# Kernel optimization log

Hardware: AMD Instinct MI355X
Metric: run time of the kernel (lower is better)

Reference implementation:

```python
import jax, jax.numpy as jnp
import numpy as np

N_NODES = 100000
N_EDGES = 1600000
IN_F = 64
OUT_F = 64
GRID_SIZE = 5
SPLINE_ORDER = 3
GRID_MIN, GRID_MAX = -1.0, 1.0
N_COEF = GRID_SIZE + SPLINE_ORDER  # 8 spline coefficients per (in,out)


def make_grid():
    # Extended knot grid, shape (IN_F, GRID_SIZE + 2*SPLINE_ORDER + 1)
    h = (GRID_MAX - GRID_MIN) / GRID_SIZE
    pts = jnp.arange(-SPLINE_ORDER, GRID_SIZE + SPLINE_ORDER + 1, dtype=jnp.float32) * h + GRID_MIN
    return jnp.tile(pts[None, :], (IN_F, 1))


def b_splines(x, grid):
    # x: (N, IN_F) -> bases: (N, IN_F, N_COEF) via Cox-de Boor recursion
    xe = x[..., None]
    bases = ((xe >= grid[:, :-1]) & (xe < grid[:, 1:])).astype(x.dtype)
    for j in range(1, SPLINE_ORDER + 1):
        left = (xe - grid[:, : -(j + 1)]) / (grid[:, j:-1] - grid[:, : -(j + 1)])
        right = (grid[:, j + 1:] - xe) / (grid[:, j + 1:] - grid[:, 1:-j])
        bases = left * bases[..., :-1] + right * bases[..., 1:]
    return bases


def kan_apply(x, base_w, spline_w, grid):
    # base path: silu(x) @ W_b^T ; spline path: flattened B-spline bases @ W_s^T
    base = jnp.matmul(jax.nn.silu(x), base_w.T)
    sp = b_splines(x, grid).reshape(x.shape[0], -1)          # (N, IN_F*N_COEF)
    spline = jnp.matmul(sp, spline_w.reshape(OUT_F, -1).T)    # (N, OUT_F)
    return base + spline


def setup_inputs() -> dict:
    key = jax.random.key(0)
    k1, k2, k3, k4, k5, k6 = jax.random.split(key, 6)
    x = jax.random.normal(k1, (N_NODES, IN_F), dtype=jnp.float32)
    edge_index = jax.random.randint(k2, (2, N_EDGES), 0, N_NODES, dtype=jnp.int32)
    s = 1.0 / np.sqrt(IN_F)
    base_w_layer = jax.random.normal(k3, (OUT_F, IN_F), dtype=jnp.float32) * s
    spline_w_layer = jax.random.normal(k4, (OUT_F, IN_F, N_COEF), dtype=jnp.float32) * 0.1 * s
    base_w_conv = jax.random.normal(k5, (OUT_F, IN_F), dtype=jnp.float32) * s
    spline_w_conv = jax.random.normal(k6, (OUT_F, IN_F, N_COEF), dtype=jnp.float32) * 0.1 * s
    return {
        "x": x,
        "base_w_layer": base_w_layer,
        "spline_w_layer": spline_w_layer,
        "base_w_conv": base_w_conv,
        "spline_w_conv": spline_w_conv,
        "edge_index": edge_index,
    }


def reference(x, base_w_layer, spline_w_layer, base_w_conv, spline_w_conv, edge_index):
    grid = make_grid()
    src, dst = edge_index[0], edge_index[1]
    # A_hat symmetric normalization: deg^{-1/2}[src] * deg^{-1/2}[dst]
    deg = jax.ops.segment_sum(jnp.ones(src.shape[0], x.dtype), dst, num_segments=N_NODES)
    dinv = jnp.where(deg > 0, jax.lax.rsqrt(jnp.maximum(deg, 1.0)), 0.0)
    coef = dinv[src] * dinv[dst]                              # (E,)
    msg = x[src] * coef[:, None]                              # (E, IN_F) gather
    agg = jax.ops.segment_sum(msg, dst, num_segments=N_NODES) # (N, IN_F) scatter-add
    # aggregate_first=True: KAN transform applied after aggregation
    h_layer = kan_apply(x, base_w_layer, spline_w_layer, grid)
    h_conv = kan_apply(agg, base_w_conv, spline_w_conv, grid)
    return h_layer + h_conv
```

## Files before the change

kernel.cpp:

```cpp
#include <hip/hip_runtime.h>
#include <math.h>

#define N_NODES 100000
#define N_EDGES 1600000
#define IN_F 64
#define OUT_F 64

#define K_SLOT 10
#define CH_IF 16
#define AST 172
#define AGH 33
#define NB 64
#define NTHR 256
#define EMAXW 448

#define NBUCK 256
#define NBUCK_USED 196
#define BSH 9
#define BCAP 9728
#define BUCK_N 512
#define EPT 8
#define EPB 2048

#define NODES_PAD 100352
#define WF_U16 (8 * 20 * 512)
#define WG_SLOTS (WF_U16 / 2)
#define CSR_CAP (NBUCK_USED * BCAP)
#define OFF_DINV 0
#define OFF_ROWPTR (OFF_DINV + NODES_PAD)
#define OFF_ROWEND (OFF_ROWPTR + NODES_PAD)
#define OFF_WT (OFF_ROWEND + NODES_PAD)
#define OFF_BF (OFF_WT + WG_SLOTS)
#define OFF_CSR (OFF_BF + 256)
#define FIXED_SLOTS (OFF_CSR + CSR_CAP)
#define XH_SLOTS (N_NODES * IN_F / 2)
#define OFF_XH FIXED_SLOTS
#define FIXED2 (FIXED_SLOTS + XH_SLOTS)
#define AGG_ELEMS (N_NODES * IN_F)

typedef __attribute__((ext_vector_type(8))) short bf16x8;
typedef __attribute__((ext_vector_type(4))) short bf16x4;
typedef __attribute__((ext_vector_type(4))) float f32x4;

__device__ __forceinline__ unsigned int bf16_rne(float v) {
    unsigned int u = __float_as_uint(v);
    u += 0x7FFFu + ((u >> 16) & 1u);
    return u >> 16;
}

__global__ __launch_bounds__(256)
void bucket_bin_kernel(const int* __restrict__ ei, int* __restrict__ bf,
                       int2* __restrict__ pairs) {
    __shared__ int lh[NBUCK];
    __shared__ int lbs[NBUCK];
    __shared__ int lgb[NBUCK];
    __shared__ int2 spair[EPB];
    __shared__ int  sdst[EPB];
    int t = threadIdx.x;
    lh[t] = 0;
    __syncthreads();
    int e0 = blockIdx.x * EPB;
    int nE = N_EDGES - e0; if (nE > EPB) nE = EPB; if (nE < 0) nE = 0;
    int d[EPT], s[EPT], lp[EPT];
#pragma unroll
    for (int k = 0; k < EPT; ++k) {
        int idx = k * 256 + t;
        bool ok = idx < nE;
        int e = e0 + idx;
        d[k] = ok ? ei[N_EDGES + e] : -1;
        s[k] = ok ? ei[e] : 0;
        lp[k] = ok ? atomicAdd(&lh[d[k] >> BSH], 1) : 0;
    }
    __syncthreads();
    int v = lh[t];
    lbs[t] = v;
    __syncthreads();
    for (int off = 1; off < NBUCK; off <<= 1) {
        int add = (t >= off) ? lbs[t - off] : 0;
        __syncthreads();
        lbs[t] += add;
        __syncthreads();
    }
    int excl = lbs[t] - v;
    if (v) {
        int r = atomicAdd(&bf[t], v);
        int cap = (t + 1) * BCAP - v;
        lgb[t] = r > cap ? cap : r;
    }
    __syncthreads();
    lbs[t] = excl;
    __syncthreads();
#pragma unroll
    for (int k = 0; k < EPT; ++k) {
        if (d[k] >= 0) {
            int b = d[k] >> BSH;
            int sp = lbs[b] + lp[k];
            spair[sp] = make_int2(d[k], s[k]);
            sdst[sp] = lgb[b] + lp[k];
        }
    }
    __syncthreads();
    for (int p = t; p < nE; p += 256) pairs[sdst[p]] = spair[p];
}

__global__ __launch_bounds__(BUCK_N)
void bucket_build_kernel(const int2* __restrict__ pairs, const int* __restrict__ bf,
                         int* __restrict__ rowptr, int* __restrict__ rowend,
                         float* __restrict__ dinv, int* __restrict__ csr,
                         const float* __restrict__ x, unsigned short* __restrict__ xh) {
    __shared__ int ldeg[BUCK_N];
    __shared__ int sb[BUCK_N];
    __shared__ int lpos[BUCK_N];
    int t = threadIdx.x;
    int b = blockIdx.x;
    int base = b * BCAP;
    int cnt = bf[b] - base;
    if (cnt > BCAP) cnt = BCAP;
    ldeg[t] = 0;
    __syncthreads();
    for (int j = t; j < cnt; j += BUCK_N) atomicAdd(&ldeg[pairs[base + j].x & (BUCK_N - 1)], 1);
    __syncthreads();
    int v = ldeg[t];
    sb[t] = v;
    __syncthreads();
    for (int off = 1; off < BUCK_N; off <<= 1) {
        int add = (t >= off) ? sb[t - off] : 0;
        __syncthreads();
        sb[t] += add;
        __syncthreads();
    }
    int excl = sb[t] - v;
    int node = (b << BSH) + t;
    if (node < N_NODES) {
        rowptr[node] = base + excl;
        rowend[node] = base + excl + v;
        dinv[node] = (v > 0) ? rsqrtf((float)v) : 0.0f;
    }
    lpos[t] = base + excl;
    __syncthreads();
    for (int j = t; j < cnt; j += BUCK_N) {
        int2 p = pairs[base + j];
        int pos = atomicAdd(&lpos[p.x & (BUCK_N - 1)], 1);
        csr[pos] = p.y;
    }
    if (xh) {
        int nodebase = b << BSH;
        for (int f = t; f < BUCK_N * 16; f += BUCK_N) {
            int nl = f >> 4;
            int nd = nodebase + nl;
            if (nd < N_NODES) {
                int dg = ldeg[nl];
                float dn = (dg > 0) ? rsqrtf((float)dg) : 0.0f;
                float4 vv = *(const float4*)&x[nd * 64 + (f & 15) * 4];
                uint2 u;
                u.x = bf16_rne(vv.x * dn) | (bf16_rne(vv.y * dn) << 16);
                u.y = bf16_rne(vv.z * dn) | (bf16_rne(vv.w * dn) << 16);
                *(uint2*)&xh[nd * 64 + (f & 15) * 4] = u;
            }
        }
    }
}

__global__ __launch_bounds__(256)
void gather_kernel(const float* __restrict__ x, const int* __restrict__ csr,
                   const int* __restrict__ rowptr, const int* __restrict__ rowend,
                   const float* __restrict__ dinv, float* __restrict__ agg) {
    int wid = (int)((blockIdx.x * 256 + threadIdx.x) >> 6);
    int lane = threadIdx.x & 63;
    if (wid >= N_NODES) return;
    int start = rowptr[wid];
    int end = rowend[wid];
    float acc = 0.0f;
    int j = start;
    for (; j + 3 < end; j += 4) {
        int s0 = csr[j], s1 = csr[j + 1], s2 = csr[j + 2], s3 = csr[j + 3];
        float a0 = x[s0 * 64 + lane] * dinv[s0];
        float a1 = x[s1 * 64 + lane] * dinv[s1];
        float a2 = x[s2 * 64 + lane] * dinv[s2];
        float a3 = x[s3 * 64 + lane] * dinv[s3];
        acc += a0 + a1 + a2 + a3;
    }
    for (; j < end; ++j) {
        int s = csr[j];
        acc += x[s * 64 + lane] * dinv[s];
    }
    agg[wid * 64 + lane] = acc * dinv[wid];
}

__global__ void deg_kernel(const int* __restrict__ ei, float* __restrict__ deg) {
    int e = blockIdx.x * blockDim.x + threadIdx.x;
    if (e < N_EDGES) atomicAdd(&deg[ei[N_EDGES + e]], 1.0f);
}
__global__ void dinv_kernel(float* __restrict__ deg) {
    int n = blockIdx.x * blockDim.x + threadIdx.x;
    if (n < N_NODES) {
        float d = deg[n];
        deg[n] = (d > 0.0f) ? rsqrtf(d) : 0.0f;
    }
}
__global__ void scatter_kernel(const float* __restrict__ x, const int* __restrict__ ei,
                               const float* __restrict__ dinv, float* __restrict__ agg) {
    long long gtid = (long long)blockIdx.x * blockDim.x + threadIdx.x;
    int wid = (int)(gtid >> 6);
    int lane = threadIdx.x & 63;
    if (wid >= N_EDGES) return;
    int s = ei[wid];
    int d = ei[N_EDGES + wid];
    float c = dinv[s] * dinv[d];
    atomicAdd(&agg[d * 64 + lane], x[s * 64 + lane] * c);
}

__global__ void wprep_kernel(const float* __restrict__ bwl, const float* __restrict__ swl,
                             const float* __restrict__ bwc, const float* __restrict__ swc,
                             unsigned short* __restrict__ Wf, int* __restrict__ bf) {
    int gid = blockIdx.x * blockDim.x + threadIdx.x;
    if (bf && gid < NBUCK) bf[gid] = gid * BCAP;
    if (gid >= WF_U16) return;
    int fr = gid >> 9;
    int lj = gid & 511;
    int lane = lj >> 3, j = lj & 7;
    int ch = fr / 20, r2 = fr - ch * 20;
    int s = r2 >> 2, t = r2 & 3;
    int o = t * 16 + (lane & 15);
    int kk = ((lane >> 4) << 3) + s * 32 + j;
    int iL = kk / K_SLOT, c = kk - iL * K_SLOT;
    int i = (ch & 3) * CH_IF + iL;
    int path = ch >> 2;
    const float* bw = path ? bwc : bwl;
    const float* sw = path ? swc : swl;
    float v = 0.0f;
    if (c == 8) v = bw[o * IN_F + i];
    else if (c < 8) v = sw[o * 512 + i * 8 + c];
    Wf[gid] = (unsigned short)bf16_rne(v);
}

__device__ __forceinline__ void write_feat(unsigned short* Arow, int iL, float v) {
    unsigned int* Au = (unsigned int*)(Arow + iL * K_SLOT);
    float sig = __builtin_amdgcn_rcpf(1.0f + __expf(-v));
    Au[0] = 0u; Au[1] = 0u; Au[2] = 0u; Au[3] = 0u;
    Au[4] = bf16_rne(v * sig);
    float s5 = (v + 2.2f) * 2.5f;
    float fm = floorf(s5);
    int m = (int)fm;
    if (m >= 0 && m <= 10) {
        float t = s5 - fm;
        float omt = 1.0f - t;
        float t2 = t * t, t3 = t2 * t;
        float n0 = omt * omt * omt * (1.0f / 6.0f);
        float n3 = t3 * (1.0f / 6.0f);
        float n1 = 0.66666666f - t2 + 0.5f * t3;
        float n2 = 1.0f - n0 - n1 - n3;
        unsigned short* As = Arow + iL * K_SLOT;
        if (m >= 3)           As[m - 3] = (unsigned short)bf16_rne(n0);
        if (m >= 2 && m <= 9) As[m - 2] = (unsigned short)bf16_rne(n1);
        if (m >= 1 && m <= 8) As[m - 1] = (unsigned short)bf16_rne(n2);
        if (m <= 7)           As[m]     = (unsigned short)bf16_rne(n3);
    }
}

__global__ __launch_bounds__(NTHR, 4)
void kan_fused_kernel(const float* __restrict__ x, const unsigned short* __restrict__ xh,
                      const int* __restrict__ csr, const int* __restrict__ rowptr,
                      const int* __restrict__ rowend, const float* __restrict__ dinv,
                      const unsigned short* __restrict__ Wf, float* __restrict__ out) {
    __shared__ __align__(16) unsigned short A_lds[NB * AST];
    __shared__ unsigned int agg_lds[NB * AGH];
    __shared__ int csr_lds[4 * EMAXW];

    int tid = threadIdx.x;
    int nbase = blockIdx.x * NB;
    int wid = tid >> 6;
    int lane = tid & 63;
    int nloc0 = (wid << 4) + (lane & 15);
    int q = lane >> 4;
    int node0 = nbase + nloc0;
    bool ok0 = node0 < N_NODES;

    const float4 z4 = make_float4(0.f, 0.f, 0.f, 0.f);
    float4 vx[4];
#pragma unroll
    for (int c = 0; c < 4; ++c)
        vx[c] = ok0 ? *(const float4*)&x[node0 * 64 + c * CH_IF + q * 4] : z4;

    int wn0 = nbase + (wid << 4);
    int s0w = 0, slenw = 0;
    int* wcsr = &csr_lds[wid * EMAXW];
    if (wn0 < N_NODES) {
        int wnL = wn0 + 15;
        if (wnL >= N_NODES) wnL = N_NODES - 1;
        s0w = rowptr[wn0];
        slenw = rowend[wnL] - s0w;
        int cap = slenw < EMAXW ? slenw : EMAXW;
        for (int i = lane; i < cap; i += 64) wcsr[i] = csr[s0w + i];
    }

    f32x4 acc[4];
#pragma unroll
    for (int t = 0; t < 4; ++t) acc[t] = (f32x4){0.f, 0.f, 0.f, 0.f};

    int kfrag = (lane >> 4) * 8;
    const unsigned short* Abase = &A_lds[nloc0 * AST + kfrag];
    unsigned short* Arow = &A_lds[nloc0 * AST];
    const bf16x8* Bbase = (const bf16x8*)Wf + lane;

    auto do_chunk = [&](int chunk) {
        float vv[4];
        if (chunk < 4) {
            vv[0] = vx[chunk].x; vv[1] = vx[chunk].y; vv[2] = vx[chunk].z; vv[3] = vx[chunk].w;
        } else {
            int b2 = (chunk - 4) * 8 + q * 2;
            unsigned u0 = agg_lds[nloc0 * AGH + b2];
            unsigned u1 = agg_lds[nloc0 * AGH + b2 + 1];
            vv[0] = __uint_as_float(u0 << 16);
            vv[1] = __uint_as_float(u0 & 0xFFFF0000u);
            vv[2] = __uint_as_float(u1 << 16);
            vv[3] = __uint_as_float(u1 & 0xFFFF0000u);
        }
#pragma unroll
        for (int jj = 0; jj < 4; ++jj) write_feat(Arow, q * 4 + jj, vv[jj]);
#pragma unroll
        for (int s = 0; s < 5; ++s) {
            bf16x4 alo = *(const bf16x4*)(Abase + s * 32);
            bf16x4 ahi = *(const bf16x4*)(Abase + s * 32 + 4);
            bf16x8 a = __builtin_shufflevector(alo, ahi, 0, 1, 2, 3, 4, 5, 6, 7);
#pragma unroll
            for (int t = 0; t < 4; ++t) {
                bf16x8 b = Bbase[((chunk * 5 + s) * 4 + t) * 64];
                acc[t] = __builtin_amdgcn_mfma_f32_16x16x32_bf16(a, b, acc[t], 0, 0, 0);
            }
        }
    };

    auto do_gather = [&]() {
        int grp8 = lane >> 3;
        int l8 = lane & 7;
        const uint4* xh128 = (const uint4*)xh;
        for (int p = 0; p < 2; ++p) {
            int nloc = (wid << 4) + (p << 3) + grp8;
            int nd = nbase + nloc;
            float a0 = 0.f, a1 = 0.f, a2 = 0.f, a3 = 0.f;
            float a4 = 0.f, a5 = 0.f, a6 = 0.f, a7 = 0.f;
            float dn = 0.f;
            if (nd < N_NODES) {
                dn = dinv[nd];
                int j = rowptr[nd] - s0w;
                int end = rowend[nd] - s0w;
                if (end <= EMAXW) {
                    for (; j + 15 < end; j += 16) {
                        int sa[16]; uint4 ua[16];
#pragma unroll
                        for (int k = 0; k < 16; ++k) sa[k] = wcsr[j + k];
#pragma unroll
                        for (int k = 0; k < 16; ++k) ua[k] = xh128[sa[k] * 8 + l8];
#pragma unroll
                        for (int k = 0; k < 16; ++k) {
                            a0 += __uint_as_float(ua[k].x << 16);
                            a1 += __uint_as_float(ua[k].x & 0xFFFF0000u);
                            a2 += __uint_as_float(ua[k].y << 16);
                            a3 += __uint_as_float(ua[k].y & 0xFFFF0000u);
                            a4 += __uint_as_float(ua[k].z << 16);
                            a5 += __uint_as_float(ua[k].z & 0xFFFF0000u);
                            a6 += __uint_as_float(ua[k].w << 16);
                            a7 += __uint_as_float(ua[k].w & 0xFFFF0000u);
                        }
                    }
                    for (; j + 3 < end; j += 4) {
                        int sb0 = wcsr[j], sb1 = wcsr[j + 1], sb2 = wcsr[j + 2], sb3 = wcsr[j + 3];
                        uint4 u0 = xh128[sb0 * 8 + l8], u1 = xh128[sb1 * 8 + l8];
                        uint4 u2 = xh128[sb2 * 8 + l8], u3 = xh128[sb3 * 8 + l8];
                        a0 += __uint_as_float(u0.x << 16) + __uint_as_float(u1.x << 16)
                            + __uint_as_float(u2.x << 16) + __uint_as_float(u3.x << 16);
                        a1 += __uint_as_float(u0.x & 0xFFFF0000u) + __uint_as_float(u1.x & 0xFFFF0000u)
                            + __uint_as_float(u2.x & 0xFFFF0000u) + __uint_as_float(u3.x & 0xFFFF0000u);
                        a2 += __uint_as_float(u0.y << 16) + __uint_as_float(u1.y << 16)
                            + __uint_as_float(u2.y << 16) + __uint_as_float(u3.y << 16);
                        a3 += __uint_as_float(u0.y & 0xFFFF0000u) + __uint_as_float(u1.y & 0xFFFF0000u)
                            + __uint_as_float(u2.y & 0xFFFF0000u) + __uint_as_float(u3.y & 0xFFFF0000u);
                        a4 += __uint_as_float(u0.z << 16) + __uint_as_float(u1.z << 16)
                            + __uint_as_float(u2.z << 16) + __uint_as_float(u3.z << 16);
                        a5 += __uint_as_float(u0.z & 0xFFFF0000u) + __uint_as_float(u1.z & 0xFFFF0000u)
                            + __uint_as_float(u2.z & 0xFFFF0000u) + __uint_as_float(u3.z & 0xFFFF0000u);
                        a6 += __uint_as_float(u0.w << 16) + __uint_as_float(u1.w << 16)
                            + __uint_as_float(u2.w << 16) + __uint_as_float(u3.w << 16);
                        a7 += __uint_as_float(u0.w & 0xFFFF0000u) + __uint_as_float(u1.w & 0xFFFF0000u)
                            + __uint_as_float(u2.w & 0xFFFF0000u) + __uint_as_float(u3.w & 0xFFFF0000u);
                    }
                    for (; j < end; ++j) {
                        uint4 u = xh128[wcsr[j] * 8 + l8];
                        a0 += __uint_as_float(u.x << 16);
                        a1 += __uint_as_float(u.x & 0xFFFF0000u);
                        a2 += __uint_as_float(u.y << 16);
                        a3 += __uint_as_float(u.y & 0xFFFF0000u);
                        a4 += __uint_as_float(u.z << 16);
                        a5 += __uint_as_float(u.z & 0xFFFF0000u);
                        a6 += __uint_as_float(u.w << 16);
                        a7 += __uint_as_float(u.w & 0xFFFF0000u);
                    }
                } else {
                    for (int g = rowptr[nd]; g < rowend[nd]; ++g) {
                        uint4 u = xh128[csr[g] * 8 + l8];
                        a0 += __uint_as_float(u.x << 16);
                        a1 += __uint_as_float(u.x & 0xFFFF0000u);
                        a2 += __uint_as_float(u.y << 16);
                        a3 += __uint_as_float(u.y & 0xFFFF0000u);
                        a4 += __uint_as_float(u.z << 16);
                        a5 += __uint_as_float(u.z & 0xFFFF0000u);
                        a6 += __uint_as_float(u.w << 16);
                        a7 += __uint_as_float(u.w & 0xFFFF0000u);
                    }
                }
            }
            int base2 = nloc * AGH + 4 * l8;
            agg_lds[base2]     = bf16_rne(a0 * dn) | (bf16_rne(a1 * dn) << 16);
            agg_lds[base2 + 1] = bf16_rne(a2 * dn) | (bf16_rne(a3 * dn) << 16);
            agg_lds[base2 + 2] = bf16_rne(a4 * dn) | (bf16_rne(a5 * dn) << 16);
            agg_lds[base2 + 3] = bf16_rne(a6 * dn) | (bf16_rne(a7 * dn) << 16);
        }
    };

    if ((blockIdx.x & 1) == 0) {
#pragma unroll
        for (int c = 0; c < 4; ++c) do_chunk(c);
        do_gather();
#pragma unroll
        for (int c = 4; c < 8; ++c) do_chunk(c);
    } else {
        do_gather();
#pragma unroll
        for (int c = 0; c < 8; ++c) do_chunk(c);
    }

#pragma unroll
    for (int t = 0; t < 4; ++t) {
#pragma unroll
        for (int r = 0; r < 4; ++r) {
            int nd = nbase + (wid << 4) + (lane >> 4) * 4 + r;
            if (nd < N_NODES) out[nd * 64 + t * 16 + (lane & 15)] = acc[t][r];
        }
    }
}

__global__ __launch_bounds__(NTHR, 8)
void kan_mfma_kernel(const float* __restrict__ x, const float* __restrict__ agg,
                     const unsigned short* __restrict__ Wf, float* __restrict__ out) {
    __shared__ __align__(16) unsigned short A_lds[NB * AST];

    int tid = threadIdx.x;
    int nbase = blockIdx.x * NB;
    int wid = tid >> 6;
    int lane = tid & 63;
    int n = tid & (NB - 1);
    int grp = wid;
    int node = nbase + n;
    bool ok = node < N_NODES;
    const float4 z4 = make_float4(0.f, 0.f, 0.f, 0.f);
    float4 vx[4], va[4];
#pragma unroll
    for (int qq = 0; qq < 4; ++qq)
        vx[qq] = ok ? *(const float4*)&x[node * 64 + qq * CH_IF + grp * 4] : z4;
#pragma unroll
    for (int qq = 0; qq < 4; ++qq)
        va[qq] = ok ? *(const float4*)&agg[node * 64 + qq * CH_IF + grp * 4] : z4;

    f32x4 acc[4];
#pragma unroll
    for (int t = 0; t < 4; ++t) acc[t] = (f32x4){0.f, 0.f, 0.f, 0.f};

    int arow = (wid << 4) + (lane & 15);
    int kfrag = (lane >> 4) * 8;
    const unsigned short* Abase = &A_lds[arow * AST + kfrag];
    const bf16x8* Bbase = (const bf16x8*)Wf + lane;

#pragma unroll
    for (int chunk = 0; chunk < 8; ++chunk) {
        const float4 v4 = (chunk < 4) ? vx[chunk] : va[chunk - 4];
        {
            float vv[4] = {v4.x, v4.y, v4.z, v4.w};
            unsigned short* Arow = &A_lds[n * AST];
#pragma unroll
            for (int jj = 0; jj < 4; ++jj) write_feat(Arow, grp * 4 + jj, vv[jj]);
        }
        __syncthreads();
        {
#pragma unroll
            for (int s = 0; s < 5; ++s) {
                bf16x4 alo = *(const bf16x4*)(Abase + s * 32);
                bf16x4 ahi = *(const bf16x4*)(Abase + s * 32 + 4);
                bf16x8 a = __builtin_shufflevector(alo, ahi, 0, 1, 2, 3, 4, 5, 6, 7);
#pragma unroll
                for (int t = 0; t < 4; ++t) {
                    bf16x8 b = Bbase[((chunk * 5 + s) * 4 + t) * 64];
                    acc[t] = __builtin_amdgcn_mfma_f32_16x16x32_bf16(a, b, acc[t], 0, 0, 0);
                }
            }
        }
        __syncthreads();
    }

#pragma unroll
    for (int t = 0; t < 4; ++t) {
#pragma unroll
        for (int r = 0; r < 4; ++r) {
            int nd = nbase + (wid << 4) + (lane >> 4) * 4 + r;
            if (nd < N_NODES) out[nd * 64 + t * 16 + (lane & 15)] = acc[t][r];
        }
    }
}

extern "C" void kernel_launch(void* const* d_in, const int* in_sizes, int n_in,
                              void* d_out, int out_size, void* d_ws, size_t ws_size,
                              hipStream_t stream) {
    const float* x   = (const float*)d_in[0];
    const float* bwl = (const float*)d_in[1];
    const float* swl = (const float*)d_in[2];
    const float* bwc = (const float*)d_in[3];
    const float* swc = (const float*)d_in[4];
    const int*   ei  = (const int*)d_in[5];
    float* out = (float*)d_out;

    float* ws = (float*)d_ws;
    float* dinv = ws + OFF_DINV;
    int* rowptr = (int*)(ws + OFF_ROWPTR);
    int* rowend = (int*)(ws + OFF_ROWEND);
    unsigned short* Wf = (unsigned short*)(ws + OFF_WT);
    int* bf = (int*)(ws + OFF_BF);
    int* csr = (int*)(ws + OFF_CSR);
    unsigned short* xh = (unsigned short*)(ws + OFF_XH);

    const bool has_csr = ws_size >= (size_t)FIXED_SLOTS * sizeof(float);
    const bool has_xh  = ws_size >= (size_t)FIXED2 * sizeof(float);
    const size_t big_base = has_xh ? (size_t)FIXED2 : (size_t)FIXED_SLOTS;
    const bool big_in_ws = ws_size >= (big_base + (size_t)AGG_ELEMS) * sizeof(float);
    float* bigbuf = (has_csr && big_in_ws) ? (ws + big_base) : out;
    int2* pairs = (int2*)bigbuf;
    float* agg = bigbuf;

    if (has_csr) {
        wprep_kernel<<<(WF_U16 + 255) / 256, 256, 0, stream>>>(bwl, swl, bwc, swc, Wf, bf);
        bucket_bin_kernel<<<(N_EDGES + EPB - 1) / EPB, 256, 0, stream>>>(ei, bf, pairs);
        bucket_build_kernel<<<NBUCK_USED, BUCK_N, 0, stream>>>(
            pairs, bf, rowptr, rowend, dinv, csr, x, has_xh ? xh : (unsigned short*)0);
        if (has_xh) {
            kan_fused_kernel<<<(N_NODES + NB - 1) / NB, NTHR, 0, stream>>>(
                x, xh, csr, rowptr, rowend, dinv, Wf, out);
        } else {
            gather_kernel<<<(N_NODES * 64 + 255) / 256, 256, 0, stream>>>(x, csr, rowptr, rowend, dinv, agg);
            kan_mfma_kernel<<<(N_NODES + NB - 1) / NB, NTHR, 0, stream>>>(x, agg, Wf, out);
        }
    } else {
        float* deg = dinv;
        hipMemsetAsync(deg, 0, (size_t)NODES_PAD * sizeof(float), stream);
        deg_kernel<<<(N_EDGES + 255) / 256, 256, 0, stream>>>(ei, deg);
        dinv_kernel<<<(N_NODES + 255) / 256, 256, 0, stream>>>(deg);
        hipMemsetAsync(agg, 0, (size_t)AGG_ELEMS * sizeof(float), stream);
        long long scatter_threads = (long long)N_EDGES * 64;
        int scatter_blocks = (int)((scatter_threads + 255) / 256);
        scatter_kernel<<<scatter_blocks, 256, 0, stream>>>(x, ei, deg, agg);
        wprep_kernel<<<(WF_U16 + 255) / 256, 256, 0, stream>>>(bwl, swl, bwc, swc, Wf, (int*)0);
        kan_mfma_kernel<<<(N_NODES + NB - 1) / NB, NTHR, 0, stream>>>(x, agg, Wf, out);
    }
}
```

Measured before the change: 132.1 us.

## Fold weight prep into bin kernel and gather node pairs as one edge stream

Removes the separate weight-prep launch by having the edge-binning kernel also convert the weights to bf16. Bucket counters are now zeroed with a memset and become relative offsets, so the build kernel reads them as counts directly. In the fused KAN kernel each 8-lane group now handles two adjacent nodes at once and walks their combined contiguous CSR range, using masked FMAs to split the sum between the two accumulators. This is meant to cut the unrolled-loop tail waste on short rows, at the cost of twice the FMA work per edge and more registers.

```diff
diff --git a/kernel.cpp b/kernel.cpp
--- a/kernel.cpp
+++ b/kernel.cpp
@@ -50,7 +50,10 @@
 
 __global__ __launch_bounds__(256)
 void bucket_bin_kernel(const int* __restrict__ ei, int* __restrict__ bf,
-                       int2* __restrict__ pairs) {
+                       int2* __restrict__ pairs,
+                       const float* __restrict__ bwl, const float* __restrict__ swl,
+                       const float* __restrict__ bwc, const float* __restrict__ swc,
+                       unsigned short* __restrict__ Wf) {
     __shared__ int lh[NBUCK];
     __shared__ int lbs[NBUCK];
     __shared__ int lgb[NBUCK];
@@ -84,8 +87,9 @@
     int excl = lbs[t] - v;
     if (v) {
         int r = atomicAdd(&bf[t], v);
+        int gb = t * BCAP + r;
         int cap = (t + 1) * BCAP - v;
-        lgb[t] = r > cap ? cap : r;
+        lgb[t] = gb > cap ? cap : gb;
     }
     __syncthreads();
     lbs[t] = excl;
@@ -101,6 +105,26 @@
     }
     __syncthreads();
     for (int p = t; p < nE; p += 256) pairs[sdst[p]] = spair[p];
+
+    int wg = blockIdx.x * 256 + t;
+    if (wg < WF_U16) {
+        int fr = wg >> 9;
+        int lj = wg & 511;
+        int lane = lj >> 3, j = lj & 7;
+        int ch = fr / 20, r2 = fr - ch * 20;
+        int sS = r2 >> 2, tt = r2 & 3;
+        int o = tt * 16 + (lane & 15);
+        int kk = ((lane >> 4) << 3) + sS * 32 + j;
+        int iL = kk / K_SLOT, c = kk - iL * K_SLOT;
+        int i = (ch & 3) * CH_IF + iL;
+        int path = ch >> 2;
+        const float* bw = path ? bwc : bwl;
+        const float* sw = path ? swc : swl;
+        float vv = 0.0f;
+        if (c == 8) vv = bw[o * IN_F + i];
+        else if (c < 8) vv = sw[o * 512 + i * 8 + c];
+        Wf[wg] = (unsigned short)bf16_rne(vv);
+    }
 }
 
 __global__ __launch_bounds__(BUCK_N)
@@ -114,7 +138,7 @@
     int t = threadIdx.x;
     int b = blockIdx.x;
     int base = b * BCAP;
-    int cnt = bf[b] - base;
+    int cnt = bf[b];
     if (cnt > BCAP) cnt = BCAP;
     ldeg[t] = 0;
     __syncthreads();
@@ -212,9 +236,8 @@
 
 __global__ void wprep_kernel(const float* __restrict__ bwl, const float* __restrict__ swl,
                              const float* __restrict__ bwc, const float* __restrict__ swc,
-                             unsigned short* __restrict__ Wf, int* __restrict__ bf) {
+                             unsigned short* __restrict__ Wf) {
     int gid = blockIdx.x * blockDim.x + threadIdx.x;
-    if (bf && gid < NBUCK) bf[gid] = gid * BCAP;
     if (gid >= WF_U16) return;
     int fr = gid >> 9;
     int lj = gid & 511;
@@ -283,13 +306,13 @@
         vx[c] = ok0 ? *(const float4*)&x[node0 * 64 + c * CH_IF + q * 4] : z4;
 
     int wn0 = nbase + (wid << 4);
-    int s0w = 0, slenw = 0;
+    int s0w = 0;
     int* wcsr = &csr_lds[wid * EMAXW];
     if (wn0 < N_NODES) {
         int wnL = wn0 + 15;
         if (wnL >= N_NODES) wnL = N_NODES - 1;
         s0w = rowptr[wn0];
-        slenw = rowend[wnL] - s0w;
+        int slenw = rowend[wnL] - s0w;
         int cap = slenw < EMAXW ? slenw : EMAXW;
         for (int i = lane; i < cap; i += 64) wcsr[i] = csr[s0w + i];
     }
@@ -332,90 +355,111 @@
     };
 
     auto do_gather = [&]() {
-        int grp8 = lane >> 3;
+        int g8 = lane >> 3;
         int l8 = lane & 7;
         const uint4* xh128 = (const uint4*)xh;
-        for (int p = 0; p < 2; ++p) {
-            int nloc = (wid << 4) + (p << 3) + grp8;
-            int nd = nbase + nloc;
-            float a0 = 0.f, a1 = 0.f, a2 = 0.f, a3 = 0.f;
-            float a4 = 0.f, a5 = 0.f, a6 = 0.f, a7 = 0.f;
-            float dn = 0.f;
-            if (nd < N_NODES) {
-                dn = dinv[nd];
-                int j = rowptr[nd] - s0w;
-                int end = rowend[nd] - s0w;
-                if (end <= EMAXW) {
-                    for (; j + 15 < end; j += 16) {
-                        int sa[16]; uint4 ua[16];
-#pragma unroll
-                        for (int k = 0; k < 16; ++k) sa[k] = wcsr[j + k];
-#pragma unroll
-                        for (int k = 0; k < 16; ++k) ua[k] = xh128[sa[k] * 8 + l8];
-#pragma unroll
-                        for (int k = 0; k < 16; ++k) {
-                            a0 += __uint_as_float(ua[k].x << 16);
-                            a1 += __uint_as_float(ua[k].x & 0xFFFF0000u);
-                            a2 += __uint_as_float(ua[k].y << 16);
-                            a3 += __uint_as_float(ua[k].y & 0xFFFF0000u);
-                            a4 += __uint_as_float(ua[k].z << 16);
-                            a5 += __uint_as_float(ua[k].z & 0xFFFF0000u);
-                            a6 += __uint_as_float(ua[k].w << 16);
-                            a7 += __uint_as_float(ua[k].w & 0xFFFF0000u);
-                        }
+        int nlocA = (wid << 4) + (g8 << 1);
+        int nlocB = nlocA + 1;
+        int ndA = nbase + nlocA;
+        int ndB = nbase + nlocB;
+        float aA[8], aB[8];
+#pragma unroll
+        for (int i = 0; i < 8; ++i) { aA[i] = 0.f; aB[i] = 0.f; }
+        float dnA = 0.f, dnB = 0.f;
+        if (ndA < N_NODES) {
+            dnA = dinv[ndA];
+            int lo = rowptr[ndA] - s0w;
+            int mid = rowend[ndA] - s0w;
+            int hi = mid;
+            if (ndB < N_NODES) { dnB = dinv[ndB]; hi = rowend[ndB] - s0w; }
+            if (hi <= EMAXW) {
+                int j = lo;
+                for (; j + 15 < hi; j += 16) {
+                    int sa[16]; uint4 ua[16];
+#pragma unroll
+                    for (int k = 0; k < 16; ++k) sa[k] = wcsr[j + k];
+#pragma unroll
+                    for (int k = 0; k < 16; ++k) ua[k] = xh128[sa[k] * 8 + l8];
+#pragma unroll
+                    for (int k = 0; k < 16; ++k) {
+                        float mA = (j + k) < mid ? 1.0f : 0.0f;
+                        float mB = 1.0f - mA;
+                        float f0 = __uint_as_float(ua[k].x << 16);
+                        float f1 = __uint_as_float(ua[k].x & 0xFFFF0000u);
+                        float f2 = __uint_as_float(ua[k].y << 16);
+                        float f3 = __uint_as_float(ua[k].y & 0xFFFF0000u);
+                        float f4 = __uint_as_float(ua[k].z << 16);
+                        float f5 = __uint_as_float(ua[k].z & 0xFFFF0000u);
+                        float f6 = __uint_as_float(ua[k].w << 16);
+                        float f7 = __uint_as_float(ua[k].w & 0xFFFF0000u);
+                        aA[0] = fmaf(mA, f0, aA[0]); aB[0] = fmaf(mB, f0, aB[0]);
+                        aA[1] = fmaf(mA, f1, aA[1]); aB[1] = fmaf(mB, f1, aB[1]);
+                        aA[2] = fmaf(mA, f2, aA[2]); aB[2] = fmaf(mB, f2, aB[2]);
+                        aA[3] = fmaf(mA, f3, aA[3]); aB[3] = fmaf(mB, f3, aB[3]);
+                        aA[4] = fmaf(mA, f4, aA[4]); aB[4] = fmaf(mB, f4, aB[4]);
+                        aA[5] = fmaf(mA, f5, aA[5]); aB[5] = fmaf(mB, f5, aB[5]);
+                        aA[6] = fmaf(mA, f6, aA[6]); aB[6] = fmaf(mB, f6, aB[6]);
+                        aA[7] = fmaf(mA, f7, aA[7]); aB[7] = fmaf(mB, f7, aB[7]);
                     }
-                    for (; j + 3 < end; j += 4) {
-                        int sb0 = wcsr[j], sb1 = wcsr[j + 1], sb2 = wcsr[j + 2], sb3 = wcsr[j + 3];
-                        uint4 u0 = xh128[sb0 * 8 + l8], u1 = xh128[sb1 * 8 + l8];
-                        uint4 u2 = xh128[sb2 * 8 + l8], u3 = xh128[sb3 * 8 + l8];
-                        a0 += __uint_as_float(u0.x << 16) + __uint_as_float(u1.x << 16)
-                            + __uint_as_float(u2.x << 16) + __uint_as_float(u3.x << 16);
-                        a1 += __uint_as_float(u0.x & 0xFFFF0000u) + __uint_as_float(u1.x & 0xFFFF0000u)
-                            + __uint_as_float(u2.x & 0xFFFF0000u) + __uint_as_float(u3.x & 0xFFFF0000u);
-                        a2 += __uint_as_float(u0.y << 16) + __uint_as_float(u1.y << 16)
-                            + __uint_as_float(u2.y << 16) + __uint_as_float(u3.y << 16);
-                        a3 += __uint_as_float(u0.y & 0xFFFF0000u) + __uint_as_float(u1.y & 0xFFFF0000u)
-                            + __uint_as_float(u2.y & 0xFFFF0000u) + __uint_as_float(u3.y & 0xFFFF0000u);
-                        a4 += __uint_as_float(u0.z << 16) + __uint_as_float(u1.z << 16)
-                            + __uint_as_float(u2.z << 16) + __uint_as_float(u3.z << 16);
-                        a5 += __uint_as_float(u0.z & 0xFFFF0000u) + __uint_as_float(u1.z & 0xFFFF0000u)
-                            + __uint_as_float(u2.z & 0xFFFF0000u) + __uint_as_float(u3.z & 0xFFFF0000u);
-                        a6 += __uint_as_float(u0.w << 16) + __uint_as_float(u1.w << 16)
-                            + __uint_as_float(u2.w << 16) + __uint_as_float(u3.w << 16);
-                        a7 += __uint_as_float(u0.w & 0xFFFF0000u) + __uint_as_float(u1.w & 0xFFFF0000u)
-                            + __uint_as_float(u2.w & 0xFFFF0000u) + __uint_as_float(u3.w & 0xFFFF0000u);
-                    }
-                    for (; j < end; ++j) {
-                        uint4 u = xh128[wcsr[j] * 8 + l8];
-                        a0 += __uint_as_float(u.x << 16);
-                        a1 += __uint_as_float(u.x & 0xFFFF0000u);
-                        a2 += __uint_as_float(u.y << 16);
-                        a3 += __uint_as_float(u.y & 0xFFFF0000u);
-                        a4 += __uint_as_float(u.z << 16);
-                        a5 += __uint_as_float(u.z & 0xFFFF0000u);
-                        a6 += __uint_as_float(u.w << 16);
-                        a7 += __uint_as_float(u.w & 0xFFFF0000u);
-                    }
-                } else {
-                    for (int g = rowptr[nd]; g < rowend[nd]; ++g) {
-                        uint4 u = xh128[csr[g] * 8 + l8];
-                        a0 += __uint_as_float(u.x << 16);
-                        a1 += __uint_as_float(u.x & 0xFFFF0000u);
-                        a2 += __uint_as_float(u.y << 16);
-                        a3 += __uint_as_float(u.y & 0xFFFF0000u);
-                        a4 += __uint_as_float(u.z << 16);
-                        a5 += __uint_as_float(u.z & 0xFFFF0000u);
-                        a6 += __uint_as_float(u.w << 16);
-                        a7 += __uint_as_float(u.w & 0xFFFF0000u);
+                }
+                for (; j < hi; ++j) {
+                    uint4 u = xh128[wcsr[j] * 8 + l8];
+                    float mA = j < mid ? 1.0f : 0.0f;
+                    float mB = 1.0f - mA;
+                    float f0 = __uint_as_float(u.x << 16);
+                    float f1 = __uint_as_float(u.x & 0xFFFF0000u);
+                    float f2 = __uint_as_float(u.y << 16);
+                    float f3 = __uint_as_float(u.y & 0xFFFF0000u);
+                    float f4 = __uint_as_float(u.z << 16);
+                    float f5 = __uint_as_float(u.z & 0xFFFF0000u);
+                    float f6 = __uint_as_float(u.w << 16);
+                    float f7 = __uint_as_float(u.w & 0xFFFF0000u);
+                    aA[0] = fmaf(mA, f0, aA[0]); aB[0] = fmaf(mB, f0, aB[0]);
+                    aA[1] = fmaf(mA, f1, aA[1]); aB[1] = fmaf(mB, f1, aB[1]);
+                    aA[2] = fmaf(mA, f2, aA[2]); aB[2] = fmaf(mB, f2, aB[2]);
+                    aA[3] = fmaf(mA, f3, aA[3]); aB[3] = fmaf(mB, f3, aB[3]);
+                    aA[4] = fmaf(mA, f4, aA[4]); aB[4] = fmaf(mB, f4, aB[4]);
+                    aA[5] = fmaf(mA, f5, aA[5]); aB[5] = fmaf(mB, f5, aB[5]);
+                    aA[6] = fmaf(mA, f6, aA[6]); aB[6] = fmaf(mB, f6, aB[6]);
+                    aA[7] = fmaf(mA, f7, aA[7]); aB[7] = fmaf(mB, f7, aB[7]);
+                }
+            } else {
+                for (int g2 = rowptr[ndA]; g2 < rowend[ndA]; ++g2) {
+                    uint4 u = xh128[csr[g2] * 8 + l8];
+                    aA[0] += __uint_as_float(u.x << 16);
+                    aA[1] += __uint_as_float(u.x & 0xFFFF0000u);
+                    aA[2] += __uint_as_float(u.y << 16);
+                    aA[3] += __uint_as_float(u.y & 0xFFFF0000u);
+                    aA[4] += __uint_as_float(u.z << 16);
+                    aA[5] += __uint_as_float(u.z & 0xFFFF0000u);
+                    aA[6] += __uint_as_float(u.w << 16);
+                    aA[7] += __uint_as_float(u.w & 0xFFFF0000u);
+                }
+                if (ndB < N_NODES) {
+                    for (int g2 = rowptr[ndB]; g2 < rowend[ndB]; ++g2) {
+                        uint4 u = xh128[csr[g2] * 8 + l8];
+                        aB[0] += __uint_as_float(u.x << 16);
+                        aB[1] += __uint_as_float(u.x & 0xFFFF0000u);
+                        aB[2] += __uint_as_float(u.y << 16);
+                        aB[3] += __uint_as_float(u.y & 0xFFFF0000u);
+                        aB[4] += __uint_as_float(u.z << 16);
+                        aB[5] += __uint_as_float(u.z & 0xFFFF0000u);
+                        aB[6] += __uint_as_float(u.w << 16);
+                        aB[7] += __uint_as_float(u.w & 0xFFFF0000u);
                     }
                 }
             }
-            int base2 = nloc * AGH + 4 * l8;
-            agg_lds[base2]     = bf16_rne(a0 * dn) | (bf16_rne(a1 * dn) << 16);
-            agg_lds[base2 + 1] = bf16_rne(a2 * dn) | (bf16_rne(a3 * dn) << 16);
-            agg_lds[base2 + 2] = bf16_rne(a4 * dn) | (bf16_rne(a5 * dn) << 16);
-            agg_lds[base2 + 3] = bf16_rne(a6 * dn) | (bf16_rne(a7 * dn) << 16);
-        }
+        }
+        int baseA = nlocA * AGH + 4 * l8;
+        agg_lds[baseA]     = bf16_rne(aA[0] * dnA) | (bf16_rne(aA[1] * dnA) << 16);
+        agg_lds[baseA + 1] = bf16_rne(aA[2] * dnA) | (bf16_rne(aA[3] * dnA) << 16);
+        agg_lds[baseA + 2] = bf16_rne(aA[4] * dnA) | (bf16_rne(aA[5] * dnA) << 16);
+        agg_lds[baseA + 3] = bf16_rne(aA[6] * dnA) | (bf16_rne(aA[7] * dnA) << 16);
+        int baseB = nlocB * AGH + 4 * l8;
+        agg_lds[baseB]     = bf16_rne(aB[0] * dnB) | (bf16_rne(aB[1] * dnB) << 16);
+        agg_lds[baseB + 1] = bf16_rne(aB[2] * dnB) | (bf16_rne(aB[3] * dnB) << 16);
+        agg_lds[baseB + 2] = bf16_rne(aB[4] * dnB) | (bf16_rne(aB[5] * dnB) << 16);
+        agg_lds[baseB + 3] = bf16_rne(aB[6] * dnB) | (bf16_rne(aB[7] * dnB) << 16);
     };
 
     if ((blockIdx.x & 1) == 0) {
@@ -536,8 +580,9 @@
     float* agg = bigbuf;
 
     if (has_csr) {
-        wprep_kernel<<<(WF_U16 + 255) / 256, 256, 0, stream>>>(bwl, swl, bwc, swc, Wf, bf);
-        bucket_bin_kernel<<<(N_EDGES + EPB - 1) / EPB, 256, 0, stream>>>(ei, bf, pairs);
+        hipMemsetAsync(bf, 0, NBUCK * sizeof(int), stream);
+        bucket_bin_kernel<<<(N_EDGES + EPB - 1) / EPB, 256, 0, stream>>>(
+            ei, bf, pairs, bwl, swl, bwc, swc, Wf);
         bucket_build_kernel<<<NBUCK_USED, BUCK_N, 0, stream>>>(
             pairs, bf, rowptr, rowend, dinv, csr, x, has_xh ? xh : (unsigned short*)0);
         if (has_xh) {
@@ -556,7 +601,7 @@
         long long scatter_threads = (long long)N_EDGES * 64;
         int scatter_blocks = (int)((scatter_threads + 255) / 256);
         scatter_kernel<<<scatter_blocks, 256, 0, stream>>>(x, ei, deg, agg);
-        wprep_kernel<<<(WF_U16 + 255) / 256, 256, 0, stream>>>(bwl, swl, bwc, swc, Wf, (int*)0);
+        wprep_kernel<<<(WF_U16 + 255) / 256, 256, 0, stream>>>(bwl, swl, bwc, swc, Wf);
         kan_mfma_kernel<<<(N_NODES + NB - 1) / NB, NTHR, 0, stream>>>(x, agg, Wf, out);
     }
 }
```

Measured after the change: 195.7 us. 1.48x slower.
